# Optimization experiments

Measured on AMD Instinct MI355X. Metric: run time of the kernel, lower is better.

The kernel has to match this reference:

```python
import jax, jax.numpy as jnp
import numpy as np

K = 1024       # vq_codebook_size
DC = 64        # vq_code_dim
BETA = 0.25    # commitment cost
DECAY = 0.99   # EMA decay
EPS = 1e-05


def setup_inputs() -> dict:
    key = jax.random.key(0)
    k1, k2, k3 = jax.random.split(key, 3)
    B, H, W = 32, 64, 64
    return {
        "z_e": jax.random.normal(k1, (B, DC, H, W), dtype=jnp.float32),
        "embedding": jax.random.normal(k2, (K, DC), dtype=jnp.float32),
        "cluster_size": jnp.ones((K,), dtype=jnp.float32),
        "embed_avg": jax.random.normal(k3, (K, DC), dtype=jnp.float32),
    }


def reference(z_e, embedding, cluster_size, embed_avg):
    B, D, H, W = z_e.shape
    # flat: [N, D] detached codes, N = B*H*W
    flat = jax.lax.stop_gradient(z_e).transpose(0, 2, 3, 1).reshape(-1, D).astype(jnp.float32)
    distances = ((flat ** 2).sum(1, keepdims=True)
                 + (embedding ** 2).sum(1)
                 - 2.0 * flat @ embedding.T)
    indices = jnp.argmin(distances, axis=-1)          # [N]
    z_q_flat = embedding[indices]                      # gather [N, D]

    # EMA statistics (training path): one-hot sums via segment_sum (scatter-add)
    counts = jax.ops.segment_sum(jnp.ones_like(indices, dtype=jnp.float32), indices, num_segments=K)
    dw = jax.ops.segment_sum(flat, indices, num_segments=K)  # encodings.T @ flat
    new_cluster_size = cluster_size * DECAY + (1.0 - DECAY) * counts
    new_embed_avg = embed_avg * DECAY + (1.0 - DECAY) * dw
    n = new_cluster_size.sum()
    smoothed = (new_cluster_size + EPS) / (n + K * EPS) * n
    new_embedding = new_embed_avg / smoothed[:, None]

    z_q = z_q_flat.reshape(B, H, W, D).transpose(0, 3, 1, 2)  # [B, D, H, W]
    commitment_loss = BETA * jnp.mean((z_e.astype(jnp.float32) - jax.lax.stop_gradient(z_q)) ** 2)
    # straight-through estimator
    z_q_st = z_e + jax.lax.stop_gradient(z_q.astype(z_e.dtype) - z_e)
    return (z_q_st, indices.reshape(B, H, W), commitment_loss,
            new_embedding, new_cluster_size, new_embed_avg)
```

## Files before the change

### kernel.cpp

```cpp
#include <hip/hip_runtime.h>

#define KCB   1024
#define DCV   64
#define HWN   4096
#define CHW   262144
#define NTOT  131072

#define O_ZQ   0
#define O_IDX  8388608
#define O_LOSS 8519680
#define O_NE   8519681
#define O_NCS  8585217
#define O_NEA  8586241

#define W_LOSS  0
#define W_CTR   64
#define W_E2    256
#define W_SM    4352
#define W_HIT   8448
#define W_LOT   139520
#define W_PARTC 270592
#define W_RLIST 401664

#define MARGIN 0.05f

typedef __attribute__((ext_vector_type(8))) short short8v;
typedef __attribute__((ext_vector_type(4))) float f32x4;

__device__ __forceinline__ unsigned short rne16(float f) {
    unsigned u = __float_as_uint(f);
    unsigned r = (u + 0x7FFFu + ((u >> 16) & 1u)) >> 16;
    return (unsigned short)r;
}

__global__ __launch_bounds__(256) void k_init(
    const float* __restrict__ emb, const float* __restrict__ ea,
    float* __restrict__ out, float* __restrict__ e2,
    short* __restrict__ hiT, short* __restrict__ loT,
    double* __restrict__ loss, int* __restrict__ ctr)
{
    int j = blockIdx.x * 256 + threadIdx.x;
    out[O_NEA + j] = 0.99f * ea[j];
    if (j < KCB) {
        const float* er = emb + j * DCV;
        float s = 0.f;
        #pragma unroll
        for (int d = 0; d < DCV; ++d) { float v = er[d]; s = fmaf(v, v, s); }
        e2[j] = s;
    }
    if (j < 8192) {
        int code = j >> 3, q = j & 7;
        const float* src = emb + code * DCV + q * 8;
        short8v h, l;
        #pragma unroll
        for (int t = 0; t < 8; ++t) {
            float x = src[t];
            unsigned short hb = rne16(x);
            float xh = __uint_as_float(((unsigned)hb) << 16);
            h[t] = (short)hb;
            l[t] = (short)rne16(x - xh);
        }
        *(short8v*)(hiT + (size_t)(q * KCB + code) * 8) = h;
        *(short8v*)(loT + (size_t)(q * KCB + code) * 8) = l;
    }
    if (j == 0) { *loss = 0.0; *ctr = 0; }
}

__global__ __launch_bounds__(256, 4) void k_dist(
    const float* __restrict__ ze, const short* __restrict__ hiT,
    const short* __restrict__ loT, const float* __restrict__ e2g,
    float* __restrict__ out, int* __restrict__ ctr, int* __restrict__ rlist)
{
    __shared__ short ldsH[8 * 128 * 8];
    __shared__ short ldsL[8 * 128 * 8];
    __shared__ float e2s[KCB];

    int tid  = threadIdx.x;
    int lane = tid & 63, w = tid >> 6;
    int g = lane >> 4, c = lane & 15;

    for (int i = tid; i < KCB; i += 256) e2s[i] = e2g[i];

    int rowbase = blockIdx.x * 128 + w * 32;
    short8v ahi[2][2], alo[2][2];
    #pragma unroll
    for (int t = 0; t < 2; ++t) {
        int n = rowbase + t * 16 + c;
        const float* base = ze + (size_t)(n >> 12) * CHW + (n & 4095);
        #pragma unroll
        for (int kh = 0; kh < 2; ++kh) {
            #pragma unroll
            for (int j = 0; j < 8; ++j) {
                int k = kh * 32 + g * 8 + j;
                float x = base[(size_t)k * HWN];
                unsigned short hb = rne16(x);
                float xh = __uint_as_float(((unsigned)hb) << 16);
                ahi[t][kh][j] = (short)hb;
                alo[t][kh][j] = (short)rne16(x - xh);
            }
        }
    }

    float best[8], second[8];
    int   bidx[8];
    #pragma unroll
    for (int i = 0; i < 8; ++i) { best[i] = 3.4e38f; second[i] = 3.4e38f; bidx[i] = 0; }

    for (int ch = 0; ch < 8; ++ch) {
        __syncthreads();
        #pragma unroll
        for (int r = 0; r < 8; ++r) {
            int u = r * 256 + tid;
            int arr = u >> 10;
            int rest = u & 1023;
            int q = rest >> 7, lc = rest & 127;
            const short* s = (arr ? loT : hiT) + (size_t)(q * KCB + ch * 128 + lc) * 8;
            short* d = (arr ? ldsL : ldsH) + rest * 8;
            *(short8v*)d = *(const short8v*)s;
        }
        __syncthreads();

        #pragma unroll 1
        for (int sub = 0; sub < 8; ++sub) {
            int boff = (sub * 16 + c) * 8;
            short8v bh0 = *(const short8v*)&ldsH[(g * 128) * 8 + boff];
            short8v bh1 = *(const short8v*)&ldsH[((4 + g) * 128) * 8 + boff];
            short8v bl0 = *(const short8v*)&ldsL[(g * 128) * 8 + boff];
            short8v bl1 = *(const short8v*)&ldsL[((4 + g) * 128) * 8 + boff];

            f32x4 a0 = {0.f, 0.f, 0.f, 0.f}, a1 = {0.f, 0.f, 0.f, 0.f};
            a0 = __builtin_amdgcn_mfma_f32_16x16x32_bf16(ahi[0][0], bh0, a0, 0, 0, 0);
            a1 = __builtin_amdgcn_mfma_f32_16x16x32_bf16(ahi[1][0], bh0, a1, 0, 0, 0);
            a0 = __builtin_amdgcn_mfma_f32_16x16x32_bf16(ahi[0][1], bh1, a0, 0, 0, 0);
            a1 = __builtin_amdgcn_mfma_f32_16x16x32_bf16(ahi[1][1], bh1, a1, 0, 0, 0);
            a0 = __builtin_amdgcn_mfma_f32_16x16x32_bf16(ahi[0][0], bl0, a0, 0, 0, 0);
            a1 = __builtin_amdgcn_mfma_f32_16x16x32_bf16(ahi[1][0], bl0, a1, 0, 0, 0);
            a0 = __builtin_amdgcn_mfma_f32_16x16x32_bf16(ahi[0][1], bl1, a0, 0, 0, 0);
            a1 = __builtin_amdgcn_mfma_f32_16x16x32_bf16(ahi[1][1], bl1, a1, 0, 0, 0);
            a0 = __builtin_amdgcn_mfma_f32_16x16x32_bf16(alo[0][0], bh0, a0, 0, 0, 0);
            a1 = __builtin_amdgcn_mfma_f32_16x16x32_bf16(alo[1][0], bh0, a1, 0, 0, 0);
            a0 = __builtin_amdgcn_mfma_f32_16x16x32_bf16(alo[0][1], bh1, a0, 0, 0, 0);
            a1 = __builtin_amdgcn_mfma_f32_16x16x32_bf16(alo[1][1], bh1, a1, 0, 0, 0);

            float e2v = e2s[ch * 128 + sub * 16 + c];
            int  code = ch * 128 + sub * 16 + c;
            #pragma unroll
            for (int t = 0; t < 2; ++t) {
                f32x4 av = t ? a1 : a0;
                #pragma unroll
                for (int r = 0; r < 4; ++r) {
                    int i = t * 4 + r;
                    float s = fmaf(-2.f, av[r], e2v);
                    bool lb = s < best[i];
                    bool ls = s < second[i];
                    second[i] = lb ? best[i] : (ls ? s : second[i]);
                    best[i]   = lb ? s : best[i];
                    bidx[i]   = lb ? code : bidx[i];
                }
            }
        }
    }

    #pragma unroll
    for (int i = 0; i < 8; ++i) {
        float b = best[i], s2 = second[i];
        int bi = bidx[i];
        #pragma unroll
        for (int m = 1; m < 16; m <<= 1) {
            float ob = __shfl_xor(b, m, 64);
            float os = __shfl_xor(s2, m, 64);
            int   oi = __shfl_xor(bi, m, 64);
            float ns = fminf(fmaxf(b, ob), fminf(s2, os));
            bi = (ob < b || (ob == b && oi < bi)) ? oi : bi;
            b  = fminf(b, ob);
            s2 = ns;
        }
        if (c == 0) {
            int t = i >> 2, r = i & 3;
            int n = rowbase + t * 16 + g * 4 + r;
            out[O_IDX + n] = (float)bi;
            if (s2 - b < MARGIN) { int p = atomicAdd(ctr, 1); rlist[p] = n; }
        }
    }
}

__global__ __launch_bounds__(256) void k_refine(
    const float* __restrict__ ze, const float* __restrict__ emb,
    float* __restrict__ out, const int* __restrict__ ctr,
    const int* __restrict__ rlist)
{
    int lane = threadIdx.x & 63;
    int gw   = (blockIdx.x * blockDim.x + threadIdx.x) >> 6;
    int nw   = (gridDim.x * blockDim.x) >> 6;
    int cnt  = *ctr;

    for (int i = gw; i < cnt; i += nw) {
        int n  = rlist[i];
        const float* zp = ze + (size_t)(n >> 12) * CHW + (n & 4095);
        float x[DCV];
        #pragma unroll
        for (int d = 0; d < DCV; ++d) x[d] = zp[(size_t)d * HWN];

        double bd = 1e300;
        int    bi = 0;
        #pragma unroll 1
        for (int cc = 0; cc < KCB / 64; ++cc) {
            int k = cc * 64 + lane;
            const float* eb = emb + k * DCV;
            double a0 = 0.0, a1 = 0.0;
            #pragma unroll
            for (int d = 0; d < DCV; d += 2) {
                double d0 = (double)x[d]     - (double)eb[d];
                double d1 = (double)x[d + 1] - (double)eb[d + 1];
                a0 = fma(d0, d0, a0);
                a1 = fma(d1, d1, a1);
            }
            double dist = a0 + a1;
            if (dist < bd || (dist == bd && k < bi)) { bd = dist; bi = k; }
        }
        #pragma unroll
        for (int off = 32; off > 0; off >>= 1) {
            double od = __shfl_xor(bd, off, 64);
            int    oi = __shfl_xor(bi, off, 64);
            if (od < bd || (od == bd && oi < bi)) { bd = od; bi = oi; }
        }
        if (lane == 0) out[O_IDX + n] = (float)bi;
    }
}

__global__ __launch_bounds__(256) void k_final(
    const float* __restrict__ ze, const float* __restrict__ emb,
    float* __restrict__ out, double* __restrict__ loss)
{
    int n  = blockIdx.x * 256 + threadIdx.x;
    int best = (int)out[O_IDX + n];

    const float* zp = ze + (size_t)(n >> 12) * CHW + (n & 4095);
    const float4* er4 = (const float4*)(emb + best * DCV);
    float er[DCV];
    #pragma unroll
    for (int q = 0; q < DCV / 4; ++q) {
        float4 v = er4[q];
        er[q * 4 + 0] = v.x; er[q * 4 + 1] = v.y;
        er[q * 4 + 2] = v.z; er[q * 4 + 3] = v.w;
    }

    float* zq = out + O_ZQ + (size_t)(n >> 12) * CHW + (n & 4095);
    float lp = 0.f;
    #pragma unroll
    for (int d = 0; d < DCV; ++d) {
        float x  = zp[(size_t)d * HWN];
        float df = x - er[d];
        lp = fmaf(df, df, lp);
        zq[(size_t)d * HWN] = x + (er[d] - x);
    }

    #pragma unroll
    for (int off = 32; off > 0; off >>= 1) lp += __shfl_down(lp, off, 64);

    __shared__ float wsum[4];
    int lane = threadIdx.x & 63, wid = threadIdx.x >> 6;
    if (lane == 0) wsum[wid] = lp;
    __syncthreads();
    if (threadIdx.x == 0) {
        double s = (double)wsum[0] + wsum[1] + wsum[2] + wsum[3];
        atomicAdd(loss, s);
    }
}

__global__ __launch_bounds__(256) void k_dw_part(
    const float* __restrict__ ze, const float* __restrict__ outIdx,
    float* __restrict__ partc, float* __restrict__ out)
{
    int gidx = blockIdx.x >> 5, b = blockIdx.x & 31;
    __shared__ float acc[8 * KCB];
    __shared__ float cnt[KCB];
    for (int i = threadIdx.x; i < 8 * KCB; i += 256) acc[i] = 0.f;
    if (gidx == 0) for (int i = threadIdx.x; i < KCB; i += 256) cnt[i] = 0.f;
    __syncthreads();

    const float* zp  = ze + (size_t)b * CHW + (size_t)gidx * 8 * HWN;
    const float* ipf = outIdx + b * HWN;
    for (int hw = threadIdx.x; hw < HWN; hw += 256) {
        int idx = (int)ipf[hw];
        #pragma unroll
        for (int i = 0; i < 8; ++i) atomicAdd(&acc[i * KCB + idx], zp[(size_t)i * HWN + hw]);
        if (gidx == 0) atomicAdd(&cnt[idx], 1.f);
    }
    __syncthreads();

    for (int j = threadIdx.x; j < 8192; j += 256) {
        int k = j >> 3, i = j & 7;
        float v = acc[i * KCB + k];
        if (v != 0.f) atomicAdd(&out[O_NEA + k * DCV + gidx * 8 + i], 0.01f * v);
    }
    if (gidx == 0)
        for (int k = threadIdx.x; k < KCB; k += 256) partc[b * KCB + k] = cnt[k];
}

__global__ __launch_bounds__(1024) void k_stats(
    const float* __restrict__ cs, const float* __restrict__ partc,
    float* __restrict__ out, float* __restrict__ sm,
    const double* __restrict__ loss)
{
    int k = threadIdx.x;
    float csum = 0.f;
    #pragma unroll
    for (int b = 0; b < 32; ++b) csum += partc[b * KCB + k];
    float ncs = fmaf(0.01f, csum, 0.99f * cs[k]);
    out[O_NCS + k] = ncs;

    __shared__ float red[KCB];
    red[k] = ncs;
    __syncthreads();
    for (int s = 512; s > 0; s >>= 1) {
        if (k < s) red[k] += red[k + s];
        __syncthreads();
    }
    float n = red[0];
    sm[k] = (ncs + 1e-5f) / (n + (float)KCB * 1e-5f) * n;
    if (k == 0) out[O_LOSS] = (float)(0.25 * (*loss) / (double)(NTOT * DCV));
}

__global__ __launch_bounds__(256) void k_embed(
    float* __restrict__ out, const float* __restrict__ sm)
{
    int j = blockIdx.x * 256 + threadIdx.x;
    out[O_NE + j] = out[O_NEA + j] / sm[j >> 6];
}

extern "C" void kernel_launch(void* const* d_in, const int* in_sizes, int n_in,
                              void* d_out, int out_size, void* d_ws, size_t ws_size,
                              hipStream_t stream)
{
    const float* ze  = (const float*)d_in[0];
    const float* emb = (const float*)d_in[1];
    const float* cs  = (const float*)d_in[2];
    const float* ea  = (const float*)d_in[3];
    float* out = (float*)d_out;

    char*   w     = (char*)d_ws;
    double* loss  = (double*)(w + W_LOSS);
    int*    ctr   = (int*)(w + W_CTR);
    float*  e2    = (float*)(w + W_E2);
    float*  sm    = (float*)(w + W_SM);
    short*  hiT   = (short*)(w + W_HIT);
    short*  loT   = (short*)(w + W_LOT);
    float*  partc = (float*)(w + W_PARTC);
    int*    rlist = (int*)(w + W_RLIST);

    k_init   <<<256, 256, 0, stream>>>(emb, ea, out, e2, hiT, loT, loss, ctr);
    k_dist   <<<1024, 256, 0, stream>>>(ze, hiT, loT, e2, out, ctr, rlist);
    k_refine <<<256, 256, 0, stream>>>(ze, emb, out, ctr, rlist);
    k_final  <<<NTOT / 256, 256, 0, stream>>>(ze, emb, out, loss);
    k_dw_part<<<256, 256, 0, stream>>>(ze, (const float*)(out + O_IDX), partc, out);
    k_stats  <<<1, 1024, 0, stream>>>(cs, partc, out, sm, loss);
    k_embed  <<<256, 256, 0, stream>>>(out, sm);
}
```

Baseline: 292.5 us.

## Tighten refine margin, transpose codebook for gathers, atomically accumulate cluster counts

Lowers the near-tie margin that sends rows to the fp64 refine pass and caps the refine list. Adds a transposed codebook so the final pass gathers per-dimension values instead of loading whole rows into registers. Cluster counts are now accumulated atomically into the output, which removes the partial-count buffer and its reduction in the stats kernel. Also simplifies the top-2 update with fminf, vectorizes refine loads, and changes the LDS accumulator layout. A smaller margin risks missing true argmin flips that bf16 split error could cause, and a full refine list silently drops rows.

```diff
diff --git a/kernel.cpp b/kernel.cpp
--- a/kernel.cpp
+++ b/kernel.cpp
@@ -19,10 +19,11 @@
 #define W_SM    4352
 #define W_HIT   8448
 #define W_LOT   139520
-#define W_PARTC 270592
-#define W_RLIST 401664
-
-#define MARGIN 0.05f
+#define W_EMBT  270592
+#define W_RLIST 532736
+
+#define RCAP   65536
+#define MARGIN 0.015f
 
 typedef __attribute__((ext_vector_type(8))) short short8v;
 typedef __attribute__((ext_vector_type(4))) float f32x4;
@@ -35,13 +36,19 @@
 
 __global__ __launch_bounds__(256) void k_init(
     const float* __restrict__ emb, const float* __restrict__ ea,
-    float* __restrict__ out, float* __restrict__ e2,
-    short* __restrict__ hiT, short* __restrict__ loT,
-    double* __restrict__ loss, int* __restrict__ ctr)
+    const float* __restrict__ cs, float* __restrict__ out,
+    float* __restrict__ e2, short* __restrict__ hiT, short* __restrict__ loT,
+    float* __restrict__ embT, double* __restrict__ loss, int* __restrict__ ctr)
 {
     int j = blockIdx.x * 256 + threadIdx.x;
     out[O_NEA + j] = 0.99f * ea[j];
+
+    {
+        int code = j >> 6, d = j & 63;
+        embT[d * KCB + code] = emb[j];
+    }
     if (j < KCB) {
+        out[O_NCS + j] = 0.99f * cs[j];
         const float* er = emb + j * DCV;
         float s = 0.f;
         #pragma unroll
@@ -152,9 +159,9 @@
                     int i = t * 4 + r;
                     float s = fmaf(-2.f, av[r], e2v);
                     bool lb = s < best[i];
-                    bool ls = s < second[i];
-                    second[i] = lb ? best[i] : (ls ? s : second[i]);
-                    best[i]   = lb ? s : best[i];
+                    float m = lb ? best[i] : s;
+                    second[i] = fminf(second[i], m);
+                    best[i]   = fminf(best[i], s);
                     bidx[i]   = lb ? code : bidx[i];
                 }
             }
@@ -179,7 +186,10 @@
             int t = i >> 2, r = i & 3;
             int n = rowbase + t * 16 + g * 4 + r;
             out[O_IDX + n] = (float)bi;
-            if (s2 - b < MARGIN) { int p = atomicAdd(ctr, 1); rlist[p] = n; }
+            if (s2 - b < MARGIN) {
+                int p = atomicAdd(ctr, 1);
+                if (p < RCAP) rlist[p] = n;
+            }
         }
     }
 }
@@ -193,9 +203,10 @@
     int gw   = (blockIdx.x * blockDim.x + threadIdx.x) >> 6;
     int nw   = (gridDim.x * blockDim.x) >> 6;
     int cnt  = *ctr;
+    if (cnt > RCAP) cnt = RCAP;
 
     for (int i = gw; i < cnt; i += nw) {
-        int n  = rlist[i];
+        int n = rlist[i];
         const float* zp = ze + (size_t)(n >> 12) * CHW + (n & 4095);
         float x[DCV];
         #pragma unroll
@@ -206,14 +217,17 @@
         #pragma unroll 1
         for (int cc = 0; cc < KCB / 64; ++cc) {
             int k = cc * 64 + lane;
-            const float* eb = emb + k * DCV;
+            const float4* eb4 = (const float4*)(emb + k * DCV);
             double a0 = 0.0, a1 = 0.0;
             #pragma unroll
-            for (int d = 0; d < DCV; d += 2) {
-                double d0 = (double)x[d]     - (double)eb[d];
-                double d1 = (double)x[d + 1] - (double)eb[d + 1];
-                a0 = fma(d0, d0, a0);
-                a1 = fma(d1, d1, a1);
+            for (int q = 0; q < DCV / 4; ++q) {
+                float4 v = eb4[q];
+                double d0 = (double)x[q * 4 + 0] - (double)v.x;
+                double d1 = (double)x[q * 4 + 1] - (double)v.y;
+                double d2 = (double)x[q * 4 + 2] - (double)v.z;
+                double d3 = (double)x[q * 4 + 3] - (double)v.w;
+                a0 = fma(d0, d0, a0); a1 = fma(d1, d1, a1);
+                a0 = fma(d2, d2, a0); a1 = fma(d3, d3, a1);
             }
             double dist = a0 + a1;
             if (dist < bd || (dist == bd && k < bi)) { bd = dist; bi = k; }
@@ -229,30 +243,27 @@
 }
 
 __global__ __launch_bounds__(256) void k_final(
-    const float* __restrict__ ze, const float* __restrict__ emb,
+    const float* __restrict__ ze, const float* __restrict__ embT,
     float* __restrict__ out, double* __restrict__ loss)
 {
-    int n  = blockIdx.x * 256 + threadIdx.x;
-    int best = (int)out[O_IDX + n];
-
-    const float* zp = ze + (size_t)(n >> 12) * CHW + (n & 4095);
-    const float4* er4 = (const float4*)(emb + best * DCV);
-    float er[DCV];
-    #pragma unroll
-    for (int q = 0; q < DCV / 4; ++q) {
-        float4 v = er4[q];
-        er[q * 4 + 0] = v.x; er[q * 4 + 1] = v.y;
-        er[q * 4 + 2] = v.z; er[q * 4 + 3] = v.w;
-    }
-
-    float* zq = out + O_ZQ + (size_t)(n >> 12) * CHW + (n & 4095);
+    int blk = blockIdx.x;
+    int b   = blk >> 4;
+    int hw  = (blk & 15) * 256 + threadIdx.x;
+    int n   = b * HWN + hw;
+
+    int myidx = (int)out[O_IDX + n];
+
+    const float* zp = ze  + (size_t)b * CHW + hw;
+    float*       zq = out + O_ZQ + (size_t)b * CHW + hw;
+
     float lp = 0.f;
-    #pragma unroll
+    #pragma unroll 8
     for (int d = 0; d < DCV; ++d) {
-        float x  = zp[(size_t)d * HWN];
-        float df = x - er[d];
+        float x = zp[(size_t)d * HWN];
+        float e = embT[d * KCB + myidx];
+        float df = x - e;
         lp = fmaf(df, df, lp);
-        zq[(size_t)d * HWN] = x + (er[d] - x);
+        zq[(size_t)d * HWN] = x + (e - x);
     }
 
     #pragma unroll
@@ -270,7 +281,7 @@
 
 __global__ __launch_bounds__(256) void k_dw_part(
     const float* __restrict__ ze, const float* __restrict__ outIdx,
-    float* __restrict__ partc, float* __restrict__ out)
+    float* __restrict__ out)
 {
     int gidx = blockIdx.x >> 5, b = blockIdx.x & 31;
     __shared__ float acc[8 * KCB];
@@ -284,32 +295,28 @@
     for (int hw = threadIdx.x; hw < HWN; hw += 256) {
         int idx = (int)ipf[hw];
         #pragma unroll
-        for (int i = 0; i < 8; ++i) atomicAdd(&acc[i * KCB + idx], zp[(size_t)i * HWN + hw]);
+        for (int i = 0; i < 8; ++i) atomicAdd(&acc[idx * 8 + i], zp[(size_t)i * HWN + hw]);
         if (gidx == 0) atomicAdd(&cnt[idx], 1.f);
     }
     __syncthreads();
 
     for (int j = threadIdx.x; j < 8192; j += 256) {
-        int k = j >> 3, i = j & 7;
-        float v = acc[i * KCB + k];
-        if (v != 0.f) atomicAdd(&out[O_NEA + k * DCV + gidx * 8 + i], 0.01f * v);
+        float v = acc[j];
+        if (v != 0.f) atomicAdd(&out[O_NEA + (j >> 3) * DCV + gidx * 8 + (j & 7)], 0.01f * v);
     }
     if (gidx == 0)
-        for (int k = threadIdx.x; k < KCB; k += 256) partc[b * KCB + k] = cnt[k];
+        for (int k = threadIdx.x; k < KCB; k += 256) {
+            float cv = cnt[k];
+            if (cv != 0.f) atomicAdd(&out[O_NCS + k], 0.01f * cv);
+        }
 }
 
 __global__ __launch_bounds__(1024) void k_stats(
-    const float* __restrict__ cs, const float* __restrict__ partc,
     float* __restrict__ out, float* __restrict__ sm,
     const double* __restrict__ loss)
 {
     int k = threadIdx.x;
-    float csum = 0.f;
-    #pragma unroll
-    for (int b = 0; b < 32; ++b) csum += partc[b * KCB + k];
-    float ncs = fmaf(0.01f, csum, 0.99f * cs[k]);
-    out[O_NCS + k] = ncs;
-
+    float ncs = out[O_NCS + k];
     __shared__ float red[KCB];
     red[k] = ncs;
     __syncthreads();
@@ -346,14 +353,14 @@
     float*  sm    = (float*)(w + W_SM);
     short*  hiT   = (short*)(w + W_HIT);
     short*  loT   = (short*)(w + W_LOT);
-    float*  partc = (float*)(w + W_PARTC);
+    float*  embT  = (float*)(w + W_EMBT);
     int*    rlist = (int*)(w + W_RLIST);
 
-    k_init   <<<256, 256, 0, stream>>>(emb, ea, out, e2, hiT, loT, loss, ctr);
+    k_init   <<<256, 256, 0, stream>>>(emb, ea, cs, out, e2, hiT, loT, embT, loss, ctr);
     k_dist   <<<1024, 256, 0, stream>>>(ze, hiT, loT, e2, out, ctr, rlist);
     k_refine <<<256, 256, 0, stream>>>(ze, emb, out, ctr, rlist);
-    k_final  <<<NTOT / 256, 256, 0, stream>>>(ze, emb, out, loss);
-    k_dw_part<<<256, 256, 0, stream>>>(ze, (const float*)(out + O_IDX), partc, out);
-    k_stats  <<<1, 1024, 0, stream>>>(cs, partc, out, sm, loss);
+    k_final  <<<512, 256, 0, stream>>>(ze, embT, out, loss);
+    k_dw_part<<<256, 256, 0, stream>>>(ze, (const float*)(out + O_IDX), out);
+    k_stats  <<<1, 1024, 0, stream>>>(out, sm, loss);
     k_embed  <<<256, 256, 0, stream>>>(out, sm);
 }
```

Measured after the change: 268.9 us. -8.1%, faster.
